# Performance work log

Measured on AMD Instinct MI355X. Metric: run time of the kernel, lower is better.

The kernel has to match this reference:

```python
import math
import jax, jax.numpy as jnp
import numpy as np

D_MODEL = 1024
SEQ_LEN = 8192
EMB_DIM = 3
ORDER = 16
BATCH = 4


def _make_pos_emb_z(seq_len, emb_dim):
    # PositionalEmbedding.__init__: t, complex-exponential bands (real+imag)
    t = np.linspace(0.0, 1.0, seq_len)[None, :, None]                      # (1, L, 1)
    bands = (emb_dim - 1) // 2                                             # = 1
    t_rescaled = np.linspace(0.0, seq_len - 1, seq_len)[None, :, None]
    w = 2 * math.pi * t_rescaled / seq_len                                 # (1, L, 1)
    f = np.linspace(1e-4, bands - 1, bands)[None, None]                    # (1, 1, bands)
    zc = np.exp(-1j * f * w)                                               # (1, L, bands)
    z = np.concatenate([t, zc.real, zc.imag], axis=-1)                     # (1, L, emb_dim)
    return jnp.asarray(z, dtype=jnp.float32)


def setup_inputs() -> dict:
    key = jax.random.key(0)
    ks = jax.random.split(key, 12)
    s_in = 1.0 / math.sqrt(EMB_DIM)
    s_h = 1.0 / math.sqrt(ORDER)
    return {
        "x": jax.random.normal(ks[0], (BATCH, D_MODEL, SEQ_LEN), dtype=jnp.float32),
        "L": SEQ_LEN,
        "z": _make_pos_emb_z(SEQ_LEN, EMB_DIM),                            # learnable pos emb
        "W1": jax.random.uniform(ks[1], (EMB_DIM, ORDER), minval=-s_in, maxval=s_in),
        "b1": jax.random.uniform(ks[2], (ORDER,), minval=-s_in, maxval=s_in),
        "W2": jax.random.uniform(ks[3], (ORDER, ORDER), minval=-s_h, maxval=s_h),
        "b2": jax.random.uniform(ks[4], (ORDER,), minval=-s_h, maxval=s_h),
        "W3": jax.random.uniform(ks[5], (ORDER, ORDER), minval=-s_h, maxval=s_h),
        "b3": jax.random.uniform(ks[6], (ORDER,), minval=-s_h, maxval=s_h),
        "Wout": jax.random.uniform(ks[7], (ORDER, D_MODEL), minval=-s_h, maxval=s_h),
        "freq": jnp.ones((1, ORDER), dtype=jnp.float32),                   # Sin freq, w=1 (shared act)
        "bias": jax.random.normal(ks[8], (D_MODEL,), dtype=jnp.float32),
    }


def _hyena_forward(x, L, z, W1, b1, W2, b2, W3, b3, Wout, freq, bias):
    # ---- implicit filter MLP (tiny) ----
    zz = z[:, :L]                                                          # (1, L, emb_dim)
    h = jnp.sin(freq * (zz @ W1 + b1))
    h = jnp.sin(freq * (h @ W2 + b2))
    h = jnp.sin(freq * (h @ W3 + b3))
    h = h @ Wout                                                           # (1, L, D)
    # ---- exponential modulation ----
    t = jnp.linspace(0.0, 1.0, SEQ_LEN, dtype=jnp.float32)[None, :, None][:, :L]
    max_decay = math.log(0.01) / 0.3
    min_decay = math.log(0.01) / 1.5
    deltas = jnp.linspace(min_decay, max_decay, D_MODEL, dtype=jnp.float32)[None, None]
    h = h * jnp.exp(-t * jnp.abs(deltas))                                  # (1, L, D)
    k = h[0].T.astype(jnp.float32)                                         # (D, L)
    # ---- FFT-based causal long convolution (safari fftconv) ----
    n = 2 * L
    xf = jnp.fft.rfft(x.astype(jnp.float32), n=n)                          # (B, D, n//2+1) complex
    kf = jnp.fft.rfft(k, n=n)                                              # (D, n//2+1)
    y = jnp.fft.irfft(xf * kf, n=n)[..., :L]                               # (B, D, L)
    return y + x * bias[:, None]


def reference(x, L, z, W1, b1, W2, b2, W3, b3, Wout, freq, bias):
    return _hyena_forward(x, L, z, W1, b1, W2, b2, W3, b3, Wout, freq, bias)
```

## Files before the change

### kernel.cpp

```cpp
#include <hip/hip_runtime.h>

#define NT 512
#define SEQ_LEN 8192

static __device__ __forceinline__ float2 f2(float x, float y){ return make_float2(x,y); }
static __device__ __forceinline__ float2 cadd(float2 a, float2 b){ return f2(a.x+b.x, a.y+b.y); }
static __device__ __forceinline__ float2 csub(float2 a, float2 b){ return f2(a.x-b.x, a.y-b.y); }
static __device__ __forceinline__ float2 cmul(float2 a, float2 b){ return f2(a.x*b.x-a.y*b.y, a.x*b.y+a.y*b.x); }
static __device__ __forceinline__ float2 cmulc(float2 a, float2 b){ return f2(a.x*b.x+a.y*b.y, a.y*b.x-a.x*b.y); }
static __device__ __forceinline__ float2 mul_mi(float2 a){ return f2(a.y, -a.x); }
static __device__ __forceinline__ float2 mul_pi(float2 a){ return f2(-a.y, a.x); }
static __device__ __forceinline__ int swz(int e){ return e ^ ((e>>4)&15) ^ ((e>>8)&15); }
static __device__ __forceinline__ int rev13(int v){ return (int)(__brev((unsigned)v) >> 19); }

__global__ void hyena_mlp(const float* __restrict__ z,
                          const float* __restrict__ W1, const float* __restrict__ b1,
                          const float* __restrict__ W2, const float* __restrict__ b2,
                          const float* __restrict__ W3, const float* __restrict__ b3,
                          const float* __restrict__ freq,
                          float* __restrict__ h3) {
    int j = blockIdx.x * blockDim.x + threadIdx.x;
    if (j >= SEQ_LEN) return;
    float z0 = z[3*j+0], z1 = z[3*j+1], z2 = z[3*j+2];
    float ha[16], hb[16];
#pragma unroll
    for (int o = 0; o < 16; ++o) {
        float acc = b1[o] + z0*W1[o] + z1*W1[16+o] + z2*W1[32+o];
        ha[o] = sinf(freq[o] * acc);
    }
#pragma unroll
    for (int p = 0; p < 16; ++p) {
        float acc = b2[p];
#pragma unroll
        for (int o = 0; o < 16; ++o) acc += ha[o] * W2[o*16+p];
        hb[p] = sinf(freq[p] * acc);
    }
#pragma unroll
    for (int q = 0; q < 16; ++q) {
        float acc = b3[q];
#pragma unroll
        for (int o = 0; o < 16; ++o) acc += hb[o] * W3[o*16+q];
        h3[j*16+q] = sinf(freq[q] * acc);
    }
}

static __device__ __forceinline__ void dif4(float2 r[16], float2 wd){
    const float2 c1 = f2(0.9238795325112867f,-0.3826834323650898f);
    const float2 c2 = f2(0.7071067811865476f,-0.7071067811865476f);
    const float2 c3 = f2(0.3826834323650898f,-0.9238795325112867f);
    float2 wc = cmul(wd,wd), wb = cmul(wc,wc), wa = cmul(wb,wb);
    float2 t0 = wd, t1 = cmul(wd,c1), t2 = cmul(wd,c2), t3 = cmul(wd,c3);
    float2 u0 = wc, u1 = cmul(wc,c2);
    { float2 u=r[0], v=r[8];  r[0]=cadd(u,v); r[8] =cmul(csub(u,v), t0); }
    { float2 u=r[1], v=r[9];  r[1]=cadd(u,v); r[9] =cmul(csub(u,v), t1); }
    { float2 u=r[2], v=r[10]; r[2]=cadd(u,v); r[10]=cmul(csub(u,v), t2); }
    { float2 u=r[3], v=r[11]; r[3]=cadd(u,v); r[11]=cmul(csub(u,v), t3); }
    { float2 u=r[4], v=r[12]; r[4]=cadd(u,v); r[12]=mul_mi(cmul(csub(u,v), t0)); }
    { float2 u=r[5], v=r[13]; r[5]=cadd(u,v); r[13]=mul_mi(cmul(csub(u,v), t1)); }
    { float2 u=r[6], v=r[14]; r[6]=cadd(u,v); r[14]=mul_mi(cmul(csub(u,v), t2)); }
    { float2 u=r[7], v=r[15]; r[7]=cadd(u,v); r[15]=mul_mi(cmul(csub(u,v), t3)); }
#pragma unroll
    for (int b = 0; b < 16; b += 8) {
        { float2 u=r[b+0], v=r[b+4]; r[b+0]=cadd(u,v); r[b+4]=cmul(csub(u,v), u0); }
        { float2 u=r[b+1], v=r[b+5]; r[b+1]=cadd(u,v); r[b+5]=cmul(csub(u,v), u1); }
        { float2 u=r[b+2], v=r[b+6]; r[b+2]=cadd(u,v); r[b+6]=mul_mi(cmul(csub(u,v), u0)); }
        { float2 u=r[b+3], v=r[b+7]; r[b+3]=cadd(u,v); r[b+7]=mul_mi(cmul(csub(u,v), u1)); }
    }
#pragma unroll
    for (int b = 0; b < 16; b += 4) {
        { float2 u=r[b+0], v=r[b+2]; r[b+0]=cadd(u,v); r[b+2]=cmul(csub(u,v), wb); }
        { float2 u=r[b+1], v=r[b+3]; r[b+1]=cadd(u,v); r[b+3]=mul_mi(cmul(csub(u,v), wb)); }
    }
#pragma unroll
    for (int b = 0; b < 16; b += 2) { float2 u=r[b], v=r[b+1]; r[b]=cadd(u,v); r[b+1]=cmul(csub(u,v), wa); }
}

static __device__ __forceinline__ void dif3(float2 r[8], float2 wd){
    const float2 c2 = f2(0.7071067811865476f,-0.7071067811865476f);
    float2 wd2 = cmul(wd,wd), wd4 = cmul(wd2,wd2);
    float2 wc2 = cmul(wd,c2);
    { float2 u=r[0], v=r[4]; r[0]=cadd(u,v); r[4]=cmul(csub(u,v), wd); }
    { float2 u=r[1], v=r[5]; r[1]=cadd(u,v); r[5]=cmul(csub(u,v), wc2); }
    { float2 u=r[2], v=r[6]; r[2]=cadd(u,v); r[6]=mul_mi(cmul(csub(u,v), wd)); }
    { float2 u=r[3], v=r[7]; r[3]=cadd(u,v); r[7]=mul_mi(cmul(csub(u,v), wc2)); }
    { float2 u=r[0], v=r[2]; r[0]=cadd(u,v); r[2]=cmul(csub(u,v), wd2); }
    { float2 u=r[1], v=r[3]; r[1]=cadd(u,v); r[3]=mul_mi(cmul(csub(u,v), wd2)); }
    { float2 u=r[4], v=r[6]; r[4]=cadd(u,v); r[6]=cmul(csub(u,v), wd2); }
    { float2 u=r[5], v=r[7]; r[5]=cadd(u,v); r[7]=mul_mi(cmul(csub(u,v), wd2)); }
    { float2 u=r[0], v=r[1]; r[0]=cadd(u,v); r[1]=cmul(csub(u,v), wd4); }
    { float2 u=r[2], v=r[3]; r[2]=cadd(u,v); r[3]=cmul(csub(u,v), wd4); }
    { float2 u=r[4], v=r[5]; r[4]=cadd(u,v); r[5]=cmul(csub(u,v), wd4); }
    { float2 u=r[6], v=r[7]; r[6]=cadd(u,v); r[7]=cmul(csub(u,v), wd4); }
}
static __device__ __forceinline__ void dit3(float2 r[8], float2 wd){
    const float2 c2 = f2(0.7071067811865476f,-0.7071067811865476f);
    float2 wd2 = cmul(wd,wd), wd4 = cmul(wd2,wd2);
    float2 wc2 = cmul(wd,c2);
    { float2 u=r[0]; float2 t=cmulc(r[1], wd4); r[0]=cadd(u,t); r[1]=csub(u,t); }
    { float2 u=r[2]; float2 t=cmulc(r[3], wd4); r[2]=cadd(u,t); r[3]=csub(u,t); }
    { float2 u=r[4]; float2 t=cmulc(r[5], wd4); r[4]=cadd(u,t); r[5]=csub(u,t); }
    { float2 u=r[6]; float2 t=cmulc(r[7], wd4); r[6]=cadd(u,t); r[7]=csub(u,t); }
    { float2 u=r[0]; float2 t=cmulc(r[2], wd2);         r[0]=cadd(u,t); r[2]=csub(u,t); }
    { float2 u=r[1]; float2 t=mul_pi(cmulc(r[3], wd2)); r[1]=cadd(u,t); r[3]=csub(u,t); }
    { float2 u=r[4]; float2 t=cmulc(r[6], wd2);         r[4]=cadd(u,t); r[6]=csub(u,t); }
    { float2 u=r[5]; float2 t=mul_pi(cmulc(r[7], wd2)); r[5]=cadd(u,t); r[7]=csub(u,t); }
    { float2 u=r[0]; float2 t=cmulc(r[4], wd);          r[0]=cadd(u,t); r[4]=csub(u,t); }
    { float2 u=r[1]; float2 t=cmulc(r[5], wc2);         r[1]=cadd(u,t); r[5]=csub(u,t); }
    { float2 u=r[2]; float2 t=mul_pi(cmulc(r[6], wd));  r[2]=cadd(u,t); r[6]=csub(u,t); }
    { float2 u=r[3]; float2 t=mul_pi(cmulc(r[7], wc2)); r[3]=cadd(u,t); r[7]=csub(u,t); }
}

static __device__ __forceinline__ void readpair(const float2* cv, int p, float2& e0, float2& e1){
    int sp = swz(p);
    float4 q = *(const float4*)&cv[sp & ~1];
    float2 lo = f2(q.x,q.y), hi = f2(q.z,q.w);
    if (sp & 1) { e0 = hi; e1 = lo; } else { e0 = lo; e1 = hi; }
}
static __device__ __forceinline__ void writepair(float2* cv, int p, float2 e0, float2 e1){
    int sp = swz(p);
    float4 q;
    if (sp & 1) q = make_float4(e1.x,e1.y,e0.x,e0.y);
    else        q = make_float4(e0.x,e0.y,e1.x,e1.y);
    *(float4*)&cv[sp & ~1] = q;
}

static __device__ __forceinline__ float2 getw(const float2* T1, const float2* T2, int k){
    return cmul(T1[k>>6], T2[k&63]);
}
static __device__ __forceinline__ float4 kpack(float2 Ck, float2 Cm, float2 w, float bds){
    const float s = 1.0f/16384.0f;
    float2 A  = f2(0.5f*(Ck.x+Cm.x), 0.5f*(Ck.y-Cm.y));
    float2 Bc = f2(0.5f*(Ck.x-Cm.x), 0.5f*(Ck.y+Cm.y));
    float2 B  = f2(Bc.y, -Bc.x);
    float2 wB = cmul(w, B);
    return make_float4((A.x+wB.x)*s + bds, (A.y+wB.y)*s,
                       (A.x-wB.x)*s + bds, -((A.y-wB.y)*s));
}
static __device__ __forceinline__ void pwmul(float2 Ck, float2 Cm, float4 Kp, float2 w,
                                             float2& Dk, float2& Dm){
    float2 A  = f2(0.5f*(Ck.x+Cm.x), 0.5f*(Ck.y-Cm.y));
    float2 Bc = f2(0.5f*(Ck.x-Cm.x), 0.5f*(Ck.y+Cm.y));
    float2 B  = f2(Bc.y, -Bc.x);
    float2 wB = cmul(w, B);
    float2 Xk = f2(A.x+wB.x, A.y+wB.y);
    float2 Xm = f2(A.x-wB.x, -(A.y-wB.y));
    float2 Yk = cmul(Xk, f2(Kp.x,Kp.y));
    float2 Ym = cmul(Xm, f2(Kp.z,Kp.w));
    float2 A2 = f2(Yk.x+Ym.x, Yk.y-Ym.y);
    float2 Bt = f2(Yk.x-Ym.x, Yk.y+Ym.y);
    float2 B2 = cmulc(Bt, w);
    Dk = f2(A2.x - B2.y, A2.y + B2.x);
    Dm = f2(A2.x + B2.y, B2.x - A2.y);
}

#define SMEMK_BYTES (8832 * 8)
__global__ __launch_bounds__(NT)
void hyena_kspec(const float* __restrict__ h3g, const float* __restrict__ Wout,
                 const float* __restrict__ bias, float4* __restrict__ A) {
    extern __shared__ float2 smem[];
    float2* cv  = smem;
    float2* tab = cv + 8192;
    float2* T1  = tab + 512;
    float2* T2  = T1 + 64;
    const int t = threadIdx.x;
    const int d = blockIdx.x;
    const float PI = 3.14159265358979323846f;

    { float s_,c_; sincosf((PI/4096.0f)*(float)t, &s_, &c_); tab[t] = f2(c_, -s_); }
    if (t < 64)       { float s_,c_; sincosf((PI/128.0f)*(float)t, &s_,&c_); T1[t] = f2(c_,-s_); }
    else if (t < 128) { int l=t-64; float s_,c_; sincosf((PI/8192.0f)*(float)l,&s_,&c_); T2[l] = f2(c_,-s_); }
    __syncthreads();

    const float2 wd1 = tab[t];
    const float2 wd2 = tab[(t&31)<<4];
    const float2 wd3 = tab[(t&1)<<8];
    const int b2 = ((t>>5)<<9) | (t&31);
    const int b3 = ((t>>1)<<5) | (t&1);

    const float dmin = -3.0701134573253941f;
    const float dmax = -15.350567286626971f;
    const float absd = fabsf(dmin + (dmax - dmin) * ((float)d * (1.0f/1023.0f)));
    const float bds = bias[d] * (1.0f/16384.0f);

    float2 r[16];
    {
        float wcol[16];
#pragma unroll
        for (int o = 0; o < 16; ++o) wcol[o] = Wout[o*1024 + d];
#pragma unroll
        for (int k = 0; k < 8; ++k) {
            int e = t + 512*k;
            const float4* h4 = (const float4*)(h3g + (size_t)(2*e)*16);
            float a0 = 0.f, a1 = 0.f;
#pragma unroll
            for (int v4 = 0; v4 < 4; ++v4) {
                float4 q0 = h4[v4], q1 = h4[4+v4];
                a0 += q0.x*wcol[4*v4] + q0.y*wcol[4*v4+1] + q0.z*wcol[4*v4+2] + q0.w*wcol[4*v4+3];
                a1 += q1.x*wcol[4*v4] + q1.y*wcol[4*v4+1] + q1.z*wcol[4*v4+2] + q1.w*wcol[4*v4+3];
            }
            float ta = (float)(2*e)   * (1.0f/8191.0f);
            float tb = (float)(2*e+1) * (1.0f/8191.0f);
            r[k] = f2(a0 * __expf(-ta*absd), a1 * __expf(-tb*absd));
        }
    }
#pragma unroll
    for (int k = 8; k < 16; ++k) r[k] = f2(0.f, 0.f);

    dif4(r, wd1);
#pragma unroll
    for (int k = 0; k < 16; ++k) cv[swz(t + 512*k)] = r[k];
    __syncthreads();
#pragma unroll
    for (int k = 0; k < 16; ++k) r[k] = cv[swz(b2 + 32*k)];
    dif4(r, wd2);
#pragma unroll
    for (int k = 0; k < 16; ++k) cv[swz(b2 + 32*k)] = r[k];
    __syncthreads();
#pragma unroll
    for (int k = 0; k < 16; ++k) r[k] = cv[swz(b3 + 2*k)];
    dif4(r, wd3);
#pragma unroll
    for (int k = 0; k < 16; ++k) cv[swz(b3 + 2*k)] = r[k];
    __syncthreads();

    float4* Ad = A + (size_t)d * 4096;
#pragma unroll 1
    for (int q = 0; q < 4; ++q) {
        int f = t + 512*q;
        if (f == 0) {
            float2 a0,a1; readpair(cv, 0, a0, a1);
            float2 C0 = cadd(a0,a1), C4 = csub(a0,a1);
            const float s = 1.0f/16384.0f;
            Ad[0] = make_float4((C0.x+C0.y)*s + bds, (C0.x-C0.y)*s + bds, C4.x*s + bds, -C4.y*s);
        } else {
            int g = 4096 - f;
            float2 a0,a1,b0,b1;
            readpair(cv, rev13(f), a0, a1);
            readpair(cv, rev13(g), b0, b1);
            float2 Cf=cadd(a0,a1), Cf4=csub(a0,a1), Cg=cadd(b0,b1), Cg4=csub(b0,b1);
            Ad[f] = kpack(Cf, Cg4, getw(T1,T2,f), bds);
            Ad[g] = kpack(Cg, Cf4, getw(T1,T2,g), bds);
        }
    }
    if (t == 0) {
        float2 b0,b1; readpair(cv, 2, b0, b1);
        Ad[2048] = kpack(cadd(b0,b1), csub(b0,b1), getw(T1,T2,2048), bds);
    }
}

#define SMEM3_BYTES (17536 * 8)
__global__ __launch_bounds__(NT, 1)
void hyena_conv3(const float4* __restrict__ A,
                 const float* __restrict__ x, float* __restrict__ out) {
    extern __shared__ float2 smem[];
    float2* cv0 = smem;
    float2* cv1 = smem + 8192;
    float2* tab = smem + 16384;
    float2* T1  = tab + 1024;
    float2* T2  = T1 + 64;
    const int t = threadIdx.x;
    const int d = blockIdx.x;
    const float PI = 3.14159265358979323846f;

#pragma unroll
    for (int i = 0; i < 2; ++i) {
        int p = t + 512*i;
        float s_,c_; sincosf((PI/4096.0f)*(float)p, &s_, &c_); tab[p] = f2(c_, -s_);
    }
    if (t < 64)       { float s_,c_; sincosf((PI/128.0f)*(float)t, &s_,&c_); T1[t] = f2(c_,-s_); }
    else if (t < 128) { int l=t-64; float s_,c_; sincosf((PI/8192.0f)*(float)l,&s_,&c_); T2[l] = f2(c_,-s_); }
    __syncthreads();

    const float2 wdB = tab[(t&127)<<3];
    const float2 wdC = tab[(t&15)<<6];
    const float2 wdD = tab[(t&1)<<9];
    const float4* Ad = A + (size_t)d * 4096;

    float2 r[8];
#pragma unroll 1
    for (int bp = 0; bp < 2; ++bp) {
#pragma unroll 1
        for (int ci = 0; ci < 2; ++ci) {
            float2* c = ci ? cv1 : cv0;
            const float2* xr = (const float2*)(x + ((size_t)(2*bp+ci)*1024 + d)*SEQ_LEN);
#pragma unroll 1
            for (int gi = 0; gi < 2; ++gi) {
                int g = t + 512*gi;
#pragma unroll
                for (int k = 0; k < 4; ++k) r[k] = xr[g + 1024*k];
#pragma unroll
                for (int k = 4; k < 8; ++k) r[k] = f2(0.f,0.f);
                dif3(r, tab[g]);
#pragma unroll
                for (int k = 0; k < 8; ++k) c[swz(g + 1024*k)] = r[k];
            }
        }
        __syncthreads();
#pragma unroll 1
        for (int ci = 0; ci < 2; ++ci) {
            float2* c = ci ? cv1 : cv0;
#pragma unroll 1
            for (int gi = 0; gi < 2; ++gi) {
                int g = t + 512*gi; int base = ((g>>7)<<10) | (g&127);
#pragma unroll
                for (int k = 0; k < 8; ++k) r[k] = c[swz(base + 128*k)];
                dif3(r, wdB);
#pragma unroll
                for (int k = 0; k < 8; ++k) c[swz(base + 128*k)] = r[k];
            }
        }
        __syncthreads();
#pragma unroll 1
        for (int ci = 0; ci < 2; ++ci) {
            float2* c = ci ? cv1 : cv0;
#pragma unroll 1
            for (int gi = 0; gi < 2; ++gi) {
                int g = t + 512*gi; int base = ((g>>4)<<7) | (g&15);
#pragma unroll
                for (int k = 0; k < 8; ++k) r[k] = c[swz(base + 16*k)];
                dif3(r, wdC);
#pragma unroll
                for (int k = 0; k < 8; ++k) c[swz(base + 16*k)] = r[k];
            }
        }
        __syncthreads();
#pragma unroll 1
        for (int ci = 0; ci < 2; ++ci) {
            float2* c = ci ? cv1 : cv0;
#pragma unroll 1
            for (int gi = 0; gi < 2; ++gi) {
                int g = t + 512*gi; int base = ((g>>1)<<4) | (g&1);
#pragma unroll
                for (int k = 0; k < 8; ++k) r[k] = c[swz(base + 2*k)];
                dif3(r, wdD);
#pragma unroll
                for (int k = 0; k < 8; ++k) c[swz(base + 2*k)] = r[k];
            }
        }
        __syncthreads();

#pragma unroll 1
        for (int q = 0; q < 4; ++q) {
            int f = t + 512*q;
            float4 Kpa = Ad[f];
            float4 Kpb = Ad[(f == 0) ? 2048 : (4096 - f)];
#pragma unroll 1
            for (int ci = 0; ci < 2; ++ci) {
                float2* c = ci ? cv1 : cv0;
                if (f == 0) {
                    float2 a0,a1; readpair(c, 0, a0, a1);
                    float2 C0 = cadd(a0,a1), C4 = csub(a0,a1);
                    float Y0 = (C0.x+C0.y) * Kpa.x, YN = (C0.x-C0.y) * Kpa.y;
                    float2 D0 = f2(Y0+YN, Y0-YN);
                    float2 Y4 = cmul(f2(C4.x,-C4.y), f2(Kpa.z, Kpa.w));
                    float2 D4 = f2(2.f*Y4.x, -2.f*Y4.y);
                    writepair(c, 0, cadd(D0,D4), csub(D0,D4));
                    float2 q0,q1; readpair(c, 2, q0, q1);
                    float2 Ck=cadd(q0,q1), Cm=csub(q0,q1), Dk, Dm;
                    pwmul(Ck, Cm, Kpb, getw(T1,T2,2048), Dk, Dm);
                    writepair(c, 2, cadd(Dk,Dm), csub(Dk,Dm));
                } else {
                    int g = 4096 - f;
                    int p1 = rev13(f), p2 = rev13(g);
                    float2 a0,a1,b0,b1;
                    readpair(c, p1, a0, a1);
                    readpair(c, p2, b0, b1);
                    float2 Cf=cadd(a0,a1), Cf4=csub(a0,a1), Cg=cadd(b0,b1), Cg4=csub(b0,b1);
                    float2 Df,Dg4,Dg,Df4;
                    pwmul(Cf, Cg4, Kpa, getw(T1,T2,f), Df, Dg4);
                    pwmul(Cg, Cf4, Kpb, getw(T1,T2,g), Dg, Df4);
                    writepair(c, p1, cadd(Df,Df4), csub(Df,Df4));
                    writepair(c, p2, cadd(Dg,Dg4), csub(Dg,Dg4));
                }
            }
        }
        __syncthreads();

#pragma unroll 1
        for (int ci = 0; ci < 2; ++ci) {
            float2* c = ci ? cv1 : cv0;
#pragma unroll 1
            for (int gi = 0; gi < 2; ++gi) {
                int g = t + 512*gi; int base = ((g>>1)<<4) | (g&1);
#pragma unroll
                for (int k = 0; k < 8; ++k) r[k] = c[swz(base + 2*k)];
                dit3(r, wdD);
#pragma unroll
                for (int k = 0; k < 8; ++k) c[swz(base + 2*k)] = r[k];
            }
        }
        __syncthreads();
#pragma unroll 1
        for (int ci = 0; ci < 2; ++ci) {
            float2* c = ci ? cv1 : cv0;
#pragma unroll 1
            for (int gi = 0; gi < 2; ++gi) {
                int g = t + 512*gi; int base = ((g>>4)<<7) | (g&15);
#pragma unroll
                for (int k = 0; k < 8; ++k) r[k] = c[swz(base + 16*k)];
                dit3(r, wdC);
#pragma unroll
                for (int k = 0; k < 8; ++k) c[swz(base + 16*k)] = r[k];
            }
        }
        __syncthreads();
#pragma unroll 1
        for (int ci = 0; ci < 2; ++ci) {
            float2* c = ci ? cv1 : cv0;
#pragma unroll 1
            for (int gi = 0; gi < 2; ++gi) {
                int g = t + 512*gi; int base = ((g>>7)<<10) | (g&127);
#pragma unroll
                for (int k = 0; k < 8; ++k) r[k] = c[swz(base + 128*k)];
                dit3(r, wdB);
#pragma unroll
                for (int k = 0; k < 8; ++k) c[swz(base + 128*k)] = r[k];
            }
        }
        __syncthreads();
#pragma unroll 1
        for (int ci = 0; ci < 2; ++ci) {
            float2* c = ci ? cv1 : cv0;
            float2* yr = (float2*)(out + ((size_t)(2*bp+ci)*1024 + d)*SEQ_LEN);
#pragma unroll 1
            for (int gi = 0; gi < 2; ++gi) {
                int g = t + 512*gi;
#pragma unroll
                for (int k = 0; k < 8; ++k) r[k] = c[swz(g + 1024*k)];
                dit3(r, tab[g]);
#pragma unroll
                for (int k = 0; k < 4; ++k) yr[g + 1024*k] = r[k];
            }
        }
        __syncthreads();
    }
}

#define SMEMF_BYTES (9348 * 8)
__global__ __launch_bounds__(NT, 2)
void hyena_conv_r10(const float* __restrict__ h3g, const float* __restrict__ Wout,
                    const float* __restrict__ x, const float* __restrict__ bias,
                    float* __restrict__ out) {
    extern __shared__ float2 smem[];
    float2* cv  = smem;
    float2* tab = cv + 8192;
    float2* T1  = tab + 1024;
    float2* T2  = T1 + 64;
    float2* Kex = T2 + 64;
    const int t = threadIdx.x;
    const int d = blockIdx.x;
    const float PI = 3.14159265358979323846f;

#pragma unroll
    for (int i = 0; i < 2; ++i) {
        int p = t + 512*i;
        float s_,c_; sincosf((PI/4096.0f)*(float)p, &s_, &c_); tab[p] = f2(c_, -s_);
    }
    if (t < 64)       { float s_,c_; sincosf((PI/128.0f)*(float)t, &s_,&c_); T1[t] = f2(c_,-s_); }
    else if (t < 128) { int l=t-64; float s_,c_; sincosf((PI/8192.0f)*(float)l,&s_,&c_); T2[l] = f2(c_,-s_); }
    __syncthreads();

    const float2 wdB = tab[(t&127)<<3];
    const float2 wdC = tab[(t&15)<<6];
    const float2 wdD = tab[(t&1)<<9];
    const float bds = bias[d] * (1.0f/16384.0f);

    float2 r[8];
#pragma unroll 1
    for (int gi = 0; gi < 2; ++gi) {
        int g = t + 512*gi;
        const float dmin = -3.0701134573253941f;
        const float dmax = -15.350567286626971f;
        const float absd = fabsf(dmin + (dmax - dmin) * ((float)d * (1.0f/1023.0f)));
#pragma unroll
        for (int k = 0; k < 4; ++k) {
            int e = g + 1024*k;
            const float4* h4 = (const float4*)(h3g + (size_t)(2*e)*16);
            float a0 = 0.f, a1 = 0.f;
#pragma unroll
            for (int v4 = 0; v4 < 4; ++v4) {
                float4 q0 = h4[v4], q1 = h4[4+v4];
                float w0 = Wout[(4*v4+0)*1024 + d], w1 = Wout[(4*v4+1)*1024 + d];
                float w2 = Wout[(4*v4+2)*1024 + d], w3 = Wout[(4*v4+3)*1024 + d];
                a0 += q0.x*w0 + q0.y*w1 + q0.z*w2 + q0.w*w3;
                a1 += q1.x*w0 + q1.y*w1 + q1.z*w2 + q1.w*w3;
            }
            float ta = (float)(2*e)   * (1.0f/8191.0f);
            float tb = (float)(2*e+1) * (1.0f/8191.0f);
            r[k] = f2(a0 * __expf(-ta*absd), a1 * __expf(-tb*absd));
        }
#pragma unroll
        for (int k = 4; k < 8; ++k) r[k] = f2(0.f, 0.f);
        dif3(r, tab[g]);
#pragma unroll
        for (int k = 0; k < 8; ++k) cv[swz(g + 1024*k)] = r[k];
    }
    __syncthreads();
#pragma unroll 1
    for (int gi = 0; gi < 2; ++gi) {
        int g = t + 512*gi; int base = ((g>>7)<<10) | (g&127);
#pragma unroll
        for (int k = 0; k < 8; ++k) r[k] = cv[swz(base + 128*k)];
        dif3(r, wdB);
#pragma unroll
        for (int k = 0; k < 8; ++k) cv[swz(base + 128*k)] = r[k];
    }
    __syncthreads();
#pragma unroll 1
    for (int gi = 0; gi < 2; ++gi) {
        int g = t + 512*gi; int base = ((g>>4)<<7) | (g&15);
#pragma unroll
        for (int k = 0; k < 8; ++k) r[k] = cv[swz(base + 16*k)];
        dif3(r, wdC);
#pragma unroll
        for (int k = 0; k < 8; ++k) cv[swz(base + 16*k)] = r[k];
    }
    __syncthreads();
#pragma unroll 1
    for (int gi = 0; gi < 2; ++gi) {
        int g = t + 512*gi; int base = ((g>>1)<<4) | (g&1);
#pragma unroll
        for (int k = 0; k < 8; ++k) r[k] = cv[swz(base + 2*k)];
        dif3(r, wdD);
#pragma unroll
        for (int k = 0; k < 8; ++k) cv[swz(base + 2*k)] = r[k];
    }
    __syncthreads();

    float4 Ka[4], Kb[4];
#pragma unroll
    for (int q = 0; q < 4; ++q) {
        int f = t + 512*q;
        if (f == 0) {
            float2 a0,a1; readpair(cv, 0, a0, a1);
            float2 C0 = cadd(a0,a1), C4 = csub(a0,a1);
            const float s = 1.0f/16384.0f;
            Ka[q] = make_float4((C0.x+C0.y)*s + bds, (C0.x-C0.y)*s + bds, C4.x*s + bds, -C4.y*s);
            Kb[q] = make_float4(0.f,0.f,0.f,0.f);
        } else {
            int g = 4096 - f;
            float2 a0,a1,b0,b1;
            readpair(cv, rev13(f), a0, a1);
            readpair(cv, rev13(g), b0, b1);
            float2 Cf=cadd(a0,a1), Cf4=csub(a0,a1), Cg=cadd(b0,b1), Cg4=csub(b0,b1);
            Ka[q] = kpack(Cf, Cg4, getw(T1,T2,f), bds);
            Kb[q] = kpack(Cg, Cf4, getw(T1,T2,g), bds);
        }
    }
    if (t == 0) {
        float2 b0,b1; readpair(cv, 2, b0, b1);
        float4 K20 = kpack(cadd(b0,b1), csub(b0,b1), getw(T1,T2,2048), bds);
        Kex[0] = f2(K20.x, K20.y);
        Kex[1] = f2(K20.z, K20.w);
    }
    __syncthreads();

#pragma unroll 1
    for (int b = 0; b < 4; ++b) {
        const float2* xr = (const float2*)(x + ((size_t)b*1024 + d)*SEQ_LEN);
        float2* yr = (float2*)(out + ((size_t)b*1024 + d)*SEQ_LEN);
#pragma unroll 1
        for (int gi = 0; gi < 2; ++gi) {
            int g = t + 512*gi;
#pragma unroll
            for (int k = 0; k < 4; ++k) r[k] = xr[g + 1024*k];
#pragma unroll
            for (int k = 4; k < 8; ++k) r[k] = f2(0.f,0.f);
            dif3(r, tab[g]);
#pragma unroll
            for (int k = 0; k < 8; ++k) cv[swz(g + 1024*k)] = r[k];
        }
        __syncthreads();
#pragma unroll 1
        for (int gi = 0; gi < 2; ++gi) {
            int g = t + 512*gi; int base = ((g>>7)<<10) | (g&127);
#pragma unroll
            for (int k = 0; k < 8; ++k) r[k] = cv[swz(base + 128*k)];
            dif3(r, wdB);
#pragma unroll
            for (int k = 0; k < 8; ++k) cv[swz(base + 128*k)] = r[k];
        }
        __syncthreads();
#pragma unroll 1
        for (int gi = 0; gi < 2; ++gi) {
            int g = t + 512*gi; int base = ((g>>4)<<7) | (g&15);
#pragma unroll
            for (int k = 0; k < 8; ++k) r[k] = cv[swz(base + 16*k)];
            dif3(r, wdC);
#pragma unroll
            for (int k = 0; k < 8; ++k) cv[swz(base + 16*k)] = r[k];
        }
        __syncthreads();
#pragma unroll 1
        for (int gi = 0; gi < 2; ++gi) {
            int g = t + 512*gi; int base = ((g>>1)<<4) | (g&1);
#pragma unroll
            for (int k = 0; k < 8; ++k) r[k] = cv[swz(base + 2*k)];
            dif3(r, wdD);
#pragma unroll
            for (int k = 0; k < 8; ++k) cv[swz(base + 2*k)] = r[k];
        }
        __syncthreads();
#pragma unroll
        for (int q = 0; q < 4; ++q) {
            int f = t + 512*q;
            if (f == 0) {
                float2 a0,a1; readpair(cv, 0, a0, a1);
                float2 C0 = cadd(a0,a1), C4 = csub(a0,a1);
                float Y0 = (C0.x+C0.y) * Ka[0].x, YN = (C0.x-C0.y) * Ka[0].y;
                float2 D0 = f2(Y0+YN, Y0-YN);
                float2 Y4 = cmul(f2(C4.x,-C4.y), f2(Ka[0].z, Ka[0].w));
                float2 D4 = f2(2.f*Y4.x, -2.f*Y4.y);
                writepair(cv, 0, cadd(D0,D4), csub(D0,D4));
            } else {
                int g = 4096 - f;
                int p1 = rev13(f), p2 = rev13(g);
                float2 a0,a1,b0,b1;
                readpair(cv, p1, a0, a1);
                readpair(cv, p2, b0, b1);
                float2 Cf=cadd(a0,a1), Cf4=csub(a0,a1), Cg=cadd(b0,b1), Cg4=csub(b0,b1);
                float2 Df,Dg4,Dg,Df4;
                pwmul(Cf, Cg4, Ka[q], getw(T1,T2,f), Df, Dg4);
                pwmul(Cg, Cf4, Kb[q], getw(T1,T2,g), Dg, Df4);
                writepair(cv, p1, cadd(Df,Df4), csub(Df,Df4));
                writepair(cv, p2, cadd(Dg,Dg4), csub(Dg,Dg4));
            }
        }
        if (t == 0) {
            float4 K20 = make_float4(Kex[0].x, Kex[0].y, Kex[1].x, Kex[1].y);
            float2 b0,b1; readpair(cv, 2, b0, b1);
            float2 Ck=cadd(b0,b1), Cm=csub(b0,b1), Dk, Dm;
            pwmul(Ck, Cm, K20, getw(T1,T2,2048), Dk, Dm);
            writepair(cv, 2, cadd(Dk,Dm), csub(Dk,Dm));
        }
        __syncthreads();
#pragma unroll 1
        for (int gi = 0; gi < 2; ++gi) {
            int g = t + 512*gi; int base = ((g>>1)<<4) | (g&1);
#pragma unroll
            for (int k = 0; k < 8; ++k) r[k] = cv[swz(base + 2*k)];
            dit3(r, wdD);
#pragma unroll
            for (int k = 0; k < 8; ++k) cv[swz(base + 2*k)] = r[k];
        }
        __syncthreads();
#pragma unroll 1
        for (int gi = 0; gi < 2; ++gi) {
            int g = t + 512*gi; int base = ((g>>4)<<7) | (g&15);
#pragma unroll
            for (int k = 0; k < 8; ++k) r[k] = cv[swz(base + 16*k)];
            dit3(r, wdC);
#pragma unroll
            for (int k = 0; k < 8; ++k) cv[swz(base + 16*k)] = r[k];
        }
        __syncthreads();
#pragma unroll 1
        for (int gi = 0; gi < 2; ++gi) {
            int g = t + 512*gi; int base = ((g>>7)<<10) | (g&127);
#pragma unroll
            for (int k = 0; k < 8; ++k) r[k] = cv[swz(base + 128*k)];
            dit3(r, wdB);
#pragma unroll
            for (int k = 0; k < 8; ++k) cv[swz(base + 128*k)] = r[k];
        }
        __syncthreads();
#pragma unroll 1
        for (int gi = 0; gi < 2; ++gi) {
            int g = t + 512*gi;
#pragma unroll
            for (int k = 0; k < 8; ++k) r[k] = cv[swz(g + 1024*k)];
            dit3(r, tab[g]);
#pragma unroll
            for (int k = 0; k < 4; ++k) yr[g + 1024*k] = r[k];
        }
        __syncthreads();
    }
}

extern "C" void kernel_launch(void* const* d_in, const int* in_sizes, int n_in,
                              void* d_out, int out_size, void* d_ws, size_t ws_size,
                              hipStream_t stream) {
    const float* x    = (const float*)d_in[0];
    const float* z    = (const float*)d_in[2];
    const float* W1   = (const float*)d_in[3];
    const float* b1   = (const float*)d_in[4];
    const float* W2   = (const float*)d_in[5];
    const float* b2   = (const float*)d_in[6];
    const float* W3   = (const float*)d_in[7];
    const float* b3   = (const float*)d_in[8];
    const float* Wout = (const float*)d_in[9];
    const float* freq = (const float*)d_in[10];
    const float* bias = (const float*)d_in[11];
    float* out = (float*)d_out;
    float* h3  = (float*)d_ws;
    float4* A  = (float4*)((char*)d_ws + 512*1024);

    const size_t need2 = 512*1024 + (size_t)1024*4096*16;

    hipLaunchKernelGGL(hyena_mlp, dim3(SEQ_LEN/256), dim3(256), 0, stream,
                       z, W1, b1, W2, b2, W3, b3, freq, h3);

    static bool attr_set = false;
    if (!attr_set) {
        (void)hipFuncSetAttribute((const void*)hyena_kspec,
                                  hipFuncAttributeMaxDynamicSharedMemorySize, SMEMK_BYTES);
        (void)hipFuncSetAttribute((const void*)hyena_conv3,
                                  hipFuncAttributeMaxDynamicSharedMemorySize, SMEM3_BYTES);
        (void)hipFuncSetAttribute((const void*)hyena_conv_r10,
                                  hipFuncAttributeMaxDynamicSharedMemorySize, SMEMF_BYTES);
        attr_set = true;
    }

    if (ws_size >= need2) {
        hipLaunchKernelGGL(hyena_kspec, dim3(1024), dim3(NT), SMEMK_BYTES, stream,
                           h3, Wout, bias, A);
        hipLaunchKernelGGL(hyena_conv3, dim3(1024), dim3(NT), SMEM3_BYTES, stream,
                           A, x, out);
    } else {
        hipLaunchKernelGGL(hyena_conv_r10, dim3(1024), dim3(NT), SMEMF_BYTES, stream,
                           h3, Wout, x, bias, out);
    }
}
```

Baseline: 379.0 us.

## Add low-LDS single-buffer conv kernel and split channels between two kernels

Adds hyena_conv5, a convolution kernel that uses one 64 KB LDS buffer and computes its twiddles in registers with sincosf instead of table lookups. It declares launch bounds for two blocks per CU so more work can be resident at once. The first 512 channels go to conv5 and the remaining 512 to the existing conv3 through a new channel offset. The split launches the two halves back to back, which may leave the GPU underfilled at the tail of each launch, and conv5 adds transcendental work and gives up conv3's double buffering.

Result: slower. 404.3 us (+6.7%).

```diff
diff --git a/kernel.cpp b/kernel.cpp
--- a/kernel.cpp
+++ b/kernel.cpp
@@ -248,10 +248,157 @@
     }
 }
 
+#define SMEM5_BYTES (8192 * 8)
+__global__ __launch_bounds__(NT, 2)
+void hyena_conv5(const float4* __restrict__ A,
+                 const float* __restrict__ x, float* __restrict__ out) {
+    extern __shared__ float2 cv[];
+    const int t = threadIdx.x;
+    const int d = blockIdx.x;
+    const float PI = 3.14159265358979323846f;
+    const float2 cpi8 = f2(0.9238795325112867f, -0.3826834323650898f);
+
+    float2 wdA0, wdB, wdC;
+    { float s_,c_; sincosf((PI/4096.0f)*(float)t, &s_,&c_);        wdA0 = f2(c_,-s_); }
+    { float s_,c_; sincosf((PI/512.0f)*(float)(t&127), &s_,&c_);   wdB  = f2(c_,-s_); }
+    { float s_,c_; sincosf((PI/64.0f)*(float)(t&15), &s_,&c_);     wdC  = f2(c_,-s_); }
+    const float2 wdA1 = cmul(wdA0, cpi8);
+    const float2 wdD  = (t&1) ? cpi8 : f2(1.f, 0.f);
+    const float4* Ad = A + (size_t)d * 4096;
+
+    float2 r[8];
+#pragma unroll 1
+    for (int b = 0; b < 4; ++b) {
+        const float2* xr = (const float2*)(x + ((size_t)b*1024 + d)*SEQ_LEN);
+        float2* yr = (float2*)(out + ((size_t)b*1024 + d)*SEQ_LEN);
+
+#pragma unroll 1
+        for (int gi = 0; gi < 2; ++gi) {
+            int g = t + 512*gi;
+#pragma unroll
+            for (int k = 0; k < 4; ++k) r[k] = xr[g + 1024*k];
+#pragma unroll
+            for (int k = 4; k < 8; ++k) r[k] = f2(0.f,0.f);
+            dif3(r, gi ? wdA1 : wdA0);
+#pragma unroll
+            for (int k = 0; k < 8; ++k) cv[swz(g + 1024*k)] = r[k];
+        }
+        __syncthreads();
+#pragma unroll 1
+        for (int gi = 0; gi < 2; ++gi) {
+            int g = t + 512*gi; int base = ((g>>7)<<10) | (g&127);
+#pragma unroll
+            for (int k = 0; k < 8; ++k) r[k] = cv[swz(base + 128*k)];
+            dif3(r, wdB);
+#pragma unroll
+            for (int k = 0; k < 8; ++k) cv[swz(base + 128*k)] = r[k];
+        }
+        __syncthreads();
+#pragma unroll 1
+        for (int gi = 0; gi < 2; ++gi) {
+            int g = t + 512*gi; int base = ((g>>4)<<7) | (g&15);
+#pragma unroll
+            for (int k = 0; k < 8; ++k) r[k] = cv[swz(base + 16*k)];
+            dif3(r, wdC);
+#pragma unroll
+            for (int k = 0; k < 8; ++k) cv[swz(base + 16*k)] = r[k];
+        }
+        __syncthreads();
+#pragma unroll 1
+        for (int gi = 0; gi < 2; ++gi) {
+            int g = t + 512*gi; int base = ((g>>1)<<4) | (g&1);
+#pragma unroll
+            for (int k = 0; k < 8; ++k) r[k] = cv[swz(base + 2*k)];
+            dif3(r, wdD);
+#pragma unroll
+            for (int k = 0; k < 8; ++k) cv[swz(base + 2*k)] = r[k];
+        }
+        __syncthreads();
+
+#pragma unroll 1
+        for (int q = 0; q < 4; ++q) {
+            int f = t + 512*q;
+            float4 Kpa = Ad[f];
+            float4 Kpb = Ad[(f == 0) ? 2048 : (4096 - f)];
+            float sw, cw; sincosf((PI/8192.0f)*(float)f, &sw, &cw);
+            float2 wf = f2(cw, -sw);
+            float2 wg = f2(sw, -cw);
+            if (f == 0) {
+                float2 a0,a1; readpair(cv, 0, a0, a1);
+                float2 C0 = cadd(a0,a1), C4 = csub(a0,a1);
+                float Y0 = (C0.x+C0.y) * Kpa.x, YN = (C0.x-C0.y) * Kpa.y;
+                float2 D0 = f2(Y0+YN, Y0-YN);
+                float2 Y4 = cmul(f2(C4.x,-C4.y), f2(Kpa.z, Kpa.w));
+                float2 D4 = f2(2.f*Y4.x, -2.f*Y4.y);
+                writepair(cv, 0, cadd(D0,D4), csub(D0,D4));
+                const float2 w2048 = f2(0.7071067811865476f, -0.7071067811865476f);
+                float2 q0,q1; readpair(cv, 2, q0, q1);
+                float2 Ck=cadd(q0,q1), Cm=csub(q0,q1), Dk, Dm;
+                pwmul(Ck, Cm, Kpb, w2048, Dk, Dm);
+                writepair(cv, 2, cadd(Dk,Dm), csub(Dk,Dm));
+            } else {
+                int g = 4096 - f;
+                int p1 = rev13(f), p2 = rev13(g);
+                float2 a0,a1,b0,b1;
+                readpair(cv, p1, a0, a1);
+                readpair(cv, p2, b0, b1);
+                float2 Cf=cadd(a0,a1), Cf4=csub(a0,a1), Cg=cadd(b0,b1), Cg4=csub(b0,b1);
+                float2 Df,Dg4,Dg,Df4;
+                pwmul(Cf, Cg4, Kpa, wf, Df, Dg4);
+                pwmul(Cg, Cf4, Kpb, wg, Dg, Df4);
+                writepair(cv, p1, cadd(Df,Df4), csub(Df,Df4));
+                writepair(cv, p2, cadd(Dg,Dg4), csub(Dg,Dg4));
+            }
+        }
+        __syncthreads();
+
+#pragma unroll 1
+        for (int gi = 0; gi < 2; ++gi) {
+            int g = t + 512*gi; int base = ((g>>1)<<4) | (g&1);
+#pragma unroll
+            for (int k = 0; k < 8; ++k) r[k] = cv[swz(base + 2*k)];
+            dit3(r, wdD);
+#pragma unroll
+            for (int k = 0; k < 8; ++k) cv[swz(base + 2*k)] = r[k];
+        }
+        __syncthreads();
+#pragma unroll 1
+        for (int gi = 0; gi < 2; ++gi) {
+            int g = t + 512*gi; int base = ((g>>4)<<7) | (g&15);
+#pragma unroll
+            for (int k = 0; k < 8; ++k) r[k] = cv[swz(base + 16*k)];
+            dit3(r, wdC);
+#pragma unroll
+            for (int k = 0; k < 8; ++k) cv[swz(base + 16*k)] = r[k];
+        }
+        __syncthreads();
+#pragma unroll 1
+        for (int gi = 0; gi < 2; ++gi) {
+            int g = t + 512*gi; int base = ((g>>7)<<10) | (g&127);
+#pragma unroll
+            for (int k = 0; k < 8; ++k) r[k] = cv[swz(base + 128*k)];
+            dit3(r, wdB);
+#pragma unroll
+            for (int k = 0; k < 8; ++k) cv[swz(base + 128*k)] = r[k];
+        }
+        __syncthreads();
+#pragma unroll 1
+        for (int gi = 0; gi < 2; ++gi) {
+            int g = t + 512*gi;
+#pragma unroll
+            for (int k = 0; k < 8; ++k) r[k] = cv[swz(g + 1024*k)];
+            dit3(r, gi ? wdA1 : wdA0);
+#pragma unroll
+            for (int k = 0; k < 4; ++k) yr[g + 1024*k] = r[k];
+        }
+        __syncthreads();
+    }
+}
+
 #define SMEM3_BYTES (17536 * 8)
 __global__ __launch_bounds__(NT, 1)
 void hyena_conv3(const float4* __restrict__ A,
-                 const float* __restrict__ x, float* __restrict__ out) {
+                 const float* __restrict__ x, float* __restrict__ out, int d0) {
     extern __shared__ float2 smem[];
     float2* cv0 = smem;
     float2* cv1 = smem + 8192;
@@ -259,7 +406,7 @@
     float2* T1  = tab + 1024;
     float2* T2  = T1 + 64;
     const int t = threadIdx.x;
-    const int d = blockIdx.x;
+    const int d = blockIdx.x + d0;
     const float PI = 3.14159265358979323846f;
 
 #pragma unroll
@@ -704,6 +851,8 @@
     if (!attr_set) {
         (void)hipFuncSetAttribute((const void*)hyena_kspec,
                                   hipFuncAttributeMaxDynamicSharedMemorySize, SMEMK_BYTES);
+        (void)hipFuncSetAttribute((const void*)hyena_conv5,
+                                  hipFuncAttributeMaxDynamicSharedMemorySize, SMEM5_BYTES);
         (void)hipFuncSetAttribute((const void*)hyena_conv3,
                                   hipFuncAttributeMaxDynamicSharedMemorySize, SMEM3_BYTES);
         (void)hipFuncSetAttribute((const void*)hyena_conv_r10,
@@ -714,8 +863,10 @@
     if (ws_size >= need2) {
         hipLaunchKernelGGL(hyena_kspec, dim3(1024), dim3(NT), SMEMK_BYTES, stream,
                            h3, Wout, bias, A);
-        hipLaunchKernelGGL(hyena_conv3, dim3(1024), dim3(NT), SMEM3_BYTES, stream,
+        hipLaunchKernelGGL(hyena_conv5, dim3(512), dim3(NT), SMEM5_BYTES, stream,
                            A, x, out);
+        hipLaunchKernelGGL(hyena_conv3, dim3(512), dim3(NT), SMEM3_BYTES, stream,
+                           A, x, out, 512);
     } else {
         hipLaunchKernelGGL(hyena_conv_r10, dim3(1024), dim3(NT), SMEMF_BYTES, stream,
                            h3, Wout, x, bias, out);
```

## Use 1024-thread blocks with single FFT buffer per batch in conv kernel

Applied to the files above, without the earlier changes.

Rewrites the convolution kernel to use 1024 threads per block. Each thread now handles one radix-8 group per stage, and the kernel processes the four batches sequentially through a single 8192-element shared buffer. Before, 512 threads looped over two groups and two buffers at once (batch pairs). This halves LDS use per block, removes the inner ci/gi loops and recomputed indices, and raises wave count per block for latency hiding. The cost is more barriers in total, since there are now four passes of syncs instead of two, and possibly higher register pressure limits at 1024 threads.

After: 597.6 us. 1.58x slower.

```diff
diff --git a/kernel.cpp b/kernel.cpp
--- a/kernel.cpp
+++ b/kernel.cpp
@@ -248,190 +248,122 @@
     }
 }
 
-#define SMEM3_BYTES (17536 * 8)
-__global__ __launch_bounds__(NT, 1)
-void hyena_conv3(const float4* __restrict__ A,
+#define SMEM8_BYTES (9344 * 8)
+__global__ __launch_bounds__(1024, 1)
+void hyena_conv8(const float4* __restrict__ A,
                  const float* __restrict__ x, float* __restrict__ out) {
     extern __shared__ float2 smem[];
-    float2* cv0 = smem;
-    float2* cv1 = smem + 8192;
-    float2* tab = smem + 16384;
+    float2* cv  = smem;
+    float2* tab = cv + 8192;
     float2* T1  = tab + 1024;
     float2* T2  = T1 + 64;
     const int t = threadIdx.x;
     const int d = blockIdx.x;
     const float PI = 3.14159265358979323846f;
 
-#pragma unroll
-    for (int i = 0; i < 2; ++i) {
-        int p = t + 512*i;
-        float s_,c_; sincosf((PI/4096.0f)*(float)p, &s_, &c_); tab[p] = f2(c_, -s_);
-    }
+    { float s_,c_; sincosf((PI/4096.0f)*(float)t, &s_, &c_); tab[t] = f2(c_, -s_); }
     if (t < 64)       { float s_,c_; sincosf((PI/128.0f)*(float)t, &s_,&c_); T1[t] = f2(c_,-s_); }
     else if (t < 128) { int l=t-64; float s_,c_; sincosf((PI/8192.0f)*(float)l,&s_,&c_); T2[l] = f2(c_,-s_); }
     __syncthreads();
 
+    const float2 wdA = tab[t];
     const float2 wdB = tab[(t&127)<<3];
     const float2 wdC = tab[(t&15)<<6];
     const float2 wdD = tab[(t&1)<<9];
+    const int bB = ((t>>7)<<10) | (t&127);
+    const int bC = ((t>>4)<<7)  | (t&15);
+    const int bD = ((t>>1)<<4)  | (t&1);
     const float4* Ad = A + (size_t)d * 4096;
 
     float2 r[8];
 #pragma unroll 1
-    for (int bp = 0; bp < 2; ++bp) {
-#pragma unroll 1
-        for (int ci = 0; ci < 2; ++ci) {
-            float2* c = ci ? cv1 : cv0;
-            const float2* xr = (const float2*)(x + ((size_t)(2*bp+ci)*1024 + d)*SEQ_LEN);
-#pragma unroll 1
-            for (int gi = 0; gi < 2; ++gi) {
-                int g = t + 512*gi;
-#pragma unroll
-                for (int k = 0; k < 4; ++k) r[k] = xr[g + 1024*k];
-#pragma unroll
-                for (int k = 4; k < 8; ++k) r[k] = f2(0.f,0.f);
-                dif3(r, tab[g]);
-#pragma unroll
-                for (int k = 0; k < 8; ++k) c[swz(g + 1024*k)] = r[k];
-            }
-        }
-        __syncthreads();
-#pragma unroll 1
-        for (int ci = 0; ci < 2; ++ci) {
-            float2* c = ci ? cv1 : cv0;
-#pragma unroll 1
-            for (int gi = 0; gi < 2; ++gi) {
-                int g = t + 512*gi; int base = ((g>>7)<<10) | (g&127);
-#pragma unroll
-                for (int k = 0; k < 8; ++k) r[k] = c[swz(base + 128*k)];
-                dif3(r, wdB);
-#pragma unroll
-                for (int k = 0; k < 8; ++k) c[swz(base + 128*k)] = r[k];
-            }
-        }
-        __syncthreads();
-#pragma unroll 1
-        for (int ci = 0; ci < 2; ++ci) {
-            float2* c = ci ? cv1 : cv0;
-#pragma unroll 1
-            for (int gi = 0; gi < 2; ++gi) {
-                int g = t + 512*gi; int base = ((g>>4)<<7) | (g&15);
-#pragma unroll
-                for (int k = 0; k < 8; ++k) r[k] = c[swz(base + 16*k)];
-                dif3(r, wdC);
-#pragma unroll
-                for (int k = 0; k < 8; ++k) c[swz(base + 16*k)] = r[k];
-            }
-        }
-        __syncthreads();
-#pragma unroll 1
-        for (int ci = 0; ci < 2; ++ci) {
-            float2* c = ci ? cv1 : cv0;
-#pragma unroll 1
-            for (int gi = 0; gi < 2; ++gi) {
-                int g = t + 512*gi; int base = ((g>>1)<<4) | (g&1);
-#pragma unroll
-                for (int k = 0; k < 8; ++k) r[k] = c[swz(base + 2*k)];
-                dif3(r, wdD);
-#pragma unroll
-                for (int k = 0; k < 8; ++k) c[swz(base + 2*k)] = r[k];
-            }
-        }
-        __syncthreads();
-
-#pragma unroll 1
-        for (int q = 0; q < 4; ++q) {
-            int f = t + 512*q;
+    for (int b = 0; b < 4; ++b) {
+        const float2* xr = (const float2*)(x + ((size_t)b*1024 + d)*SEQ_LEN);
+        float2* yr = (float2*)(out + ((size_t)b*1024 + d)*SEQ_LEN);
+
+#pragma unroll
+        for (int k = 0; k < 4; ++k) r[k] = xr[t + 1024*k];
+#pragma unroll
+        for (int k = 4; k < 8; ++k) r[k] = f2(0.f,0.f);
+        dif3(r, wdA);
+#pragma unroll
+        for (int k = 0; k < 8; ++k) cv[swz(t + 1024*k)] = r[k];
+        __syncthreads();
+#pragma unroll
+        for (int k = 0; k < 8; ++k) r[k] = cv[swz(bB + 128*k)];
+        dif3(r, wdB);
+#pragma unroll
+        for (int k = 0; k < 8; ++k) cv[swz(bB + 128*k)] = r[k];
+        __syncthreads();
+#pragma unroll
+        for (int k = 0; k < 8; ++k) r[k] = cv[swz(bC + 16*k)];
+        dif3(r, wdC);
+#pragma unroll
+        for (int k = 0; k < 8; ++k) cv[swz(bC + 16*k)] = r[k];
+        __syncthreads();
+#pragma unroll
+        for (int k = 0; k < 8; ++k) r[k] = cv[swz(bD + 2*k)];
+        dif3(r, wdD);
+#pragma unroll
+        for (int k = 0; k < 8; ++k) cv[swz(bD + 2*k)] = r[k];
+        __syncthreads();
+
+#pragma unroll 1
+        for (int q = 0; q < 2; ++q) {
+            int f = t + 1024*q;
             float4 Kpa = Ad[f];
             float4 Kpb = Ad[(f == 0) ? 2048 : (4096 - f)];
-#pragma unroll 1
-            for (int ci = 0; ci < 2; ++ci) {
-                float2* c = ci ? cv1 : cv0;
-                if (f == 0) {
-                    float2 a0,a1; readpair(c, 0, a0, a1);
-                    float2 C0 = cadd(a0,a1), C4 = csub(a0,a1);
-                    float Y0 = (C0.x+C0.y) * Kpa.x, YN = (C0.x-C0.y) * Kpa.y;
-                    float2 D0 = f2(Y0+YN, Y0-YN);
-                    float2 Y4 = cmul(f2(C4.x,-C4.y), f2(Kpa.z, Kpa.w));
-                    float2 D4 = f2(2.f*Y4.x, -2.f*Y4.y);
-                    writepair(c, 0, cadd(D0,D4), csub(D0,D4));
-                    float2 q0,q1; readpair(c, 2, q0, q1);
-                    float2 Ck=cadd(q0,q1), Cm=csub(q0,q1), Dk, Dm;
-                    pwmul(Ck, Cm, Kpb, getw(T1,T2,2048), Dk, Dm);
-                    writepair(c, 2, cadd(Dk,Dm), csub(Dk,Dm));
-                } else {
-                    int g = 4096 - f;
-                    int p1 = rev13(f), p2 = rev13(g);
-                    float2 a0,a1,b0,b1;
-                    readpair(c, p1, a0, a1);
-                    readpair(c, p2, b0, b1);
-                    float2 Cf=cadd(a0,a1), Cf4=csub(a0,a1), Cg=cadd(b0,b1), Cg4=csub(b0,b1);
-                    float2 Df,Dg4,Dg,Df4;
-                    pwmul(Cf, Cg4, Kpa, getw(T1,T2,f), Df, Dg4);
-                    pwmul(Cg, Cf4, Kpb, getw(T1,T2,g), Dg, Df4);
-                    writepair(c, p1, cadd(Df,Df4), csub(Df,Df4));
-                    writepair(c, p2, cadd(Dg,Dg4), csub(Dg,Dg4));
-                }
+            if (f == 0) {
+                float2 a0,a1; readpair(cv, 0, a0, a1);
+                float2 C0 = cadd(a0,a1), C4 = csub(a0,a1);
+                float Y0 = (C0.x+C0.y) * Kpa.x, YN = (C0.x-C0.y) * Kpa.y;
+                float2 D0 = f2(Y0+YN, Y0-YN);
+                float2 Y4 = cmul(f2(C4.x,-C4.y), f2(Kpa.z, Kpa.w));
+                float2 D4 = f2(2.f*Y4.x, -2.f*Y4.y);
+                writepair(cv, 0, cadd(D0,D4), csub(D0,D4));
+                float2 q0,q1; readpair(cv, 2, q0, q1);
+                float2 Ck=cadd(q0,q1), Cm=csub(q0,q1), Dk, Dm;
+                pwmul(Ck, Cm, Kpb, getw(T1,T2,2048), Dk, Dm);
+                writepair(cv, 2, cadd(Dk,Dm), csub(Dk,Dm));
+            } else {
+                int g = 4096 - f;
+                int p1 = rev13(f), p2 = rev13(g);
+                float2 a0,a1,b0,b1;
+                readpair(cv, p1, a0, a1);
+                readpair(cv, p2, b0, b1);
+                float2 Cf=cadd(a0,a1), Cf4=csub(a0,a1), Cg=cadd(b0,b1), Cg4=csub(b0,b1);
+                float2 Df,Dg4,Dg,Df4;
+                pwmul(Cf, Cg4, Kpa, getw(T1,T2,f), Df, Dg4);
+                pwmul(Cg, Cf4, Kpb, getw(T1,T2,g), Dg, Df4);
+                writepair(cv, p1, cadd(Df,Df4), csub(Df,Df4));
+                writepair(cv, p2, cadd(Dg,Dg4), csub(Dg,Dg4));
             }
         }
         __syncthreads();
 
-#pragma unroll 1
-        for (int ci = 0; ci < 2; ++ci) {
-            float2* c = ci ? cv1 : cv0;
-#pragma unroll 1
-            for (int gi = 0; gi < 2; ++gi) {
-                int g = t + 512*gi; int base = ((g>>1)<<4) | (g&1);
-#pragma unroll
-                for (int k = 0; k < 8; ++k) r[k] = c[swz(base + 2*k)];
-                dit3(r, wdD);
-#pragma unroll
-                for (int k = 0; k < 8; ++k) c[swz(base + 2*k)] = r[k];
-            }
-        }
-        __syncthreads();
-#pragma unroll 1
-        for (int ci = 0; ci < 2; ++ci) {
-            float2* c = ci ? cv1 : cv0;
-#pragma unroll 1
-            for (int gi = 0; gi < 2; ++gi) {
-                int g = t + 512*gi; int base = ((g>>4)<<7) | (g&15);
-#pragma unroll
-                for (int k = 0; k < 8; ++k) r[k] = c[swz(base + 16*k)];
-                dit3(r, wdC);
-#pragma unroll
-                for (int k = 0; k < 8; ++k) c[swz(base + 16*k)] = r[k];
-            }
-        }
-        __syncthreads();
-#pragma unroll 1
-        for (int ci = 0; ci < 2; ++ci) {
-            float2* c = ci ? cv1 : cv0;
-#pragma unroll 1
-            for (int gi = 0; gi < 2; ++gi) {
-                int g = t + 512*gi; int base = ((g>>7)<<10) | (g&127);
-#pragma unroll
-                for (int k = 0; k < 8; ++k) r[k] = c[swz(base + 128*k)];
-                dit3(r, wdB);
-#pragma unroll
-                for (int k = 0; k < 8; ++k) c[swz(base + 128*k)] = r[k];
-            }
-        }
-        __syncthreads();
-#pragma unroll 1
-        for (int ci = 0; ci < 2; ++ci) {
-            float2* c = ci ? cv1 : cv0;
-            float2* yr = (float2*)(out + ((size_t)(2*bp+ci)*1024 + d)*SEQ_LEN);
-#pragma unroll 1
-            for (int gi = 0; gi < 2; ++gi) {
-                int g = t + 512*gi;
-#pragma unroll
-                for (int k = 0; k < 8; ++k) r[k] = c[swz(g + 1024*k)];
-                dit3(r, tab[g]);
-#pragma unroll
-                for (int k = 0; k < 4; ++k) yr[g + 1024*k] = r[k];
-            }
-        }
+#pragma unroll
+        for (int k = 0; k < 8; ++k) r[k] = cv[swz(bD + 2*k)];
+        dit3(r, wdD);
+#pragma unroll
+        for (int k = 0; k < 8; ++k) cv[swz(bD + 2*k)] = r[k];
+        __syncthreads();
+#pragma unroll
+        for (int k = 0; k < 8; ++k) r[k] = cv[swz(bC + 16*k)];
+        dit3(r, wdC);
+#pragma unroll
+        for (int k = 0; k < 8; ++k) cv[swz(bC + 16*k)] = r[k];
+        __syncthreads();
+#pragma unroll
+        for (int k = 0; k < 8; ++k) r[k] = cv[swz(bB + 128*k)];
+        dit3(r, wdB);
+#pragma unroll
+        for (int k = 0; k < 8; ++k) cv[swz(bB + 128*k)] = r[k];
+        __syncthreads();
+#pragma unroll
+        for (int k = 0; k < 8; ++k) r[k] = cv[swz(t + 1024*k)];
+        dit3(r, wdA);
+#pragma unroll
+        for (int k = 0; k < 4; ++k) yr[t + 1024*k] = r[k];
         __syncthreads();
     }
 }
@@ -704,8 +636,8 @@
     if (!attr_set) {
         (void)hipFuncSetAttribute((const void*)hyena_kspec,
                                   hipFuncAttributeMaxDynamicSharedMemorySize, SMEMK_BYTES);
-        (void)hipFuncSetAttribute((const void*)hyena_conv3,
-                                  hipFuncAttributeMaxDynamicSharedMemorySize, SMEM3_BYTES);
+        (void)hipFuncSetAttribute((const void*)hyena_conv8,
+                                  hipFuncAttributeMaxDynamicSharedMemorySize, SMEM8_BYTES);
         (void)hipFuncSetAttribute((const void*)hyena_conv_r10,
                                   hipFuncAttributeMaxDynamicSharedMemorySize, SMEMF_BYTES);
         attr_set = true;
@@ -714,7 +646,7 @@
     if (ws_size >= need2) {
         hipLaunchKernelGGL(hyena_kspec, dim3(1024), dim3(NT), SMEMK_BYTES, stream,
                            h3, Wout, bias, A);
-        hipLaunchKernelGGL(hyena_conv3, dim3(1024), dim3(NT), SMEM3_BYTES, stream,
+        hipLaunchKernelGGL(hyena_conv8, dim3(1024), dim3(1024), SMEM8_BYTES, stream,
                            A, x, out);
     } else {
         hipLaunchKernelGGL(hyena_conv_r10, dim3(1024), dim3(NT), SMEMF_BYTES, stream,
```
